# Optimization experiments

Hardware: AMD Instinct MI355X
Metric: run time of the kernel (lower is better)

Reference implementation:

```python
import jax, jax.numpy as jnp
import numpy as np

B, T, C = 2, 2048, 1024
NUM_HEADS = 16
HEAD_DIM = C // NUM_HEADS
TEMP = 1.0
LN_EPS = 1e-6


def setup_inputs() -> dict:
    key = jax.random.key(0)
    kx, kqw, kpw = jax.random.split(key, 3)
    x = jax.random.normal(kx, (B, T, C), dtype=jnp.float32)
    # causal mask, broadcastable to [B, H, T, T]
    mask = jnp.tril(jnp.ones((T, T), dtype=bool))[None, None, :, :]
    # LayerNorm params (flax defaults: scale=1, bias=0)
    ln_scale = jnp.ones((C,), dtype=jnp.float32)
    ln_bias = jnp.zeros((C,), dtype=jnp.float32)
    # xavier_uniform init for dense kernels, zero bias (torch_linear)
    lim_qkv = float(np.sqrt(6.0 / (C + 3 * C)))
    qkv_w = jax.random.uniform(kqw, (C, 3 * C), jnp.float32, -lim_qkv, lim_qkv)
    qkv_b = jnp.zeros((3 * C,), dtype=jnp.float32)
    lim_p = float(np.sqrt(6.0 / (C + C)))
    proj_w = jax.random.uniform(kpw, (C, C), jnp.float32, -lim_p, lim_p)
    proj_b = jnp.zeros((C,), dtype=jnp.float32)
    return {"x": x, "mask": mask, "ln_scale": ln_scale, "ln_bias": ln_bias,
            "qkv_w": qkv_w, "qkv_b": qkv_b, "proj_w": proj_w, "proj_b": proj_b}


def reference(x, mask, ln_scale, ln_bias, qkv_w, qkv_b, proj_w, proj_b):
    b, t, c = x.shape
    # LayerNorm (eps=1e-6, flax default)
    mu = jnp.mean(x, axis=-1, keepdims=True)
    var = jnp.mean(jnp.square(x - mu), axis=-1, keepdims=True)
    xn = (x - mu) * jax.lax.rsqrt(var + LN_EPS) * ln_scale + ln_bias
    # fused QKV projection
    qkv = xn @ qkv_w + qkv_b
    q, k, v = jnp.split(qkv, 3, axis=-1)
    q = q.reshape(b, t, NUM_HEADS, HEAD_DIM) / TEMP
    k = k.reshape(b, t, NUM_HEADS, HEAD_DIM)
    v = v.reshape(b, t, NUM_HEADS, HEAD_DIM)
    # scaled dot-product attention with mask (eval path: no dropout)
    q = q / jnp.sqrt(jnp.float32(HEAD_DIM)).astype(x.dtype)
    scores = jnp.einsum('bqhd,bkhd->bhqk', q, k)  # [B,H,T,T]
    big_neg = jnp.finfo(x.dtype).min
    scores = jnp.where(mask, scores, big_neg)
    attn_weights = jax.nn.softmax(scores, axis=-1).astype(x.dtype)
    out = jnp.einsum('bhqk,bkhd->bqhd', attn_weights, v).reshape(b, t, c)
    return out @ proj_w + proj_b
```

## Files before the change

### kernel.cpp

```cpp
#include <hip/hip_runtime.h>
#include <cstdint>
#include <math.h>

#define DEV __device__ __forceinline__

typedef unsigned int u32;
typedef unsigned short u16;
typedef __attribute__((ext_vector_type(4))) float f32x4;
typedef __attribute__((ext_vector_type(4))) u32 u32x4;
typedef __attribute__((ext_vector_type(2))) u32 u32x2;
typedef __attribute__((ext_vector_type(8))) __bf16 bf16x8;

static_assert(sizeof(bf16x8) == 16, "bf16x8 must be 16B");

static constexpr int Tn = 2048, Cn = 1024;
static constexpr float QSCALE2 = 0.125f * 1.44269504088896f;

DEV u16 f2bf_rne(float f) {
  u32 u = __builtin_bit_cast(u32, f);
  u32 r = u + 0x7fffu + ((u >> 16) & 1u);
  return (u16)(r >> 16);
}
DEV float bf2f(u16 h) {
  u32 u = ((u32)h) << 16;
  return __builtin_bit_cast(float, u);
}
DEV u32 pack2bf(float a, float b) {
  return (u32)f2bf_rne(a) | ((u32)f2bf_rne(b) << 16);
}
DEV float fexp2(float x) {
#if __has_builtin(__builtin_amdgcn_exp2f)
  return __builtin_amdgcn_exp2f(x);
#else
  return exp2f(x);
#endif
}

DEV void stage16(const void* g, void* l) {
#if __has_builtin(__builtin_amdgcn_global_load_lds)
  __builtin_amdgcn_global_load_lds(
      (__attribute__((address_space(1))) u32*)(uintptr_t)g,
      (__attribute__((address_space(3))) u32*)l, 16, 0, 0);
#else
  *(u32x4*)l = *(const u32x4*)g;
#endif
}

__global__ __launch_bounds__(256) void pre_kernel(const float* __restrict__ x,
                                                  const float* __restrict__ sc,
                                                  const float* __restrict__ bi,
                                                  u16* __restrict__ xn,
                                                  const float* __restrict__ qkv_w,
                                                  u16* __restrict__ wqkv,
                                                  const float* __restrict__ proj_w,
                                                  u16* __restrict__ wproj) {
  __shared__ float shm[32 * 33];
  int t = threadIdx.x;
  if (blockIdx.x < 4096) {
    int row = blockIdx.x;
    const float* xr = x + (size_t)row * Cn;
    f32x4 v = *(const f32x4*)(xr + t * 4);
    float s = v.x + v.y + v.z + v.w;
    float s2 = v.x * v.x + v.y * v.y + v.z * v.z + v.w * v.w;
#pragma unroll
    for (int off = 1; off < 64; off <<= 1) {
      s += __shfl_xor(s, off);
      s2 += __shfl_xor(s2, off);
    }
    if ((t & 63) == 0) {
      shm[(t >> 6) * 2] = s;
      shm[(t >> 6) * 2 + 1] = s2;
    }
    __syncthreads();
    s = shm[0] + shm[2] + shm[4] + shm[6];
    s2 = shm[1] + shm[3] + shm[5] + shm[7];
    float mean = s * (1.0f / Cn);
    float var = s2 * (1.0f / Cn) - mean * mean;
    float rstd = rsqrtf(var + 1e-6f);
    f32x4 g = *(const f32x4*)(sc + t * 4);
    f32x4 b = *(const f32x4*)(bi + t * 4);
    u32 lo = pack2bf((v.x - mean) * rstd * g.x + b.x, (v.y - mean) * rstd * g.y + b.y);
    u32 hi = pack2bf((v.z - mean) * rstd * g.z + b.z, (v.w - mean) * rstd * g.w + b.w);
    u32x2 pack = {lo, hi};
    *(u32x2*)(xn + (size_t)row * Cn + t * 4) = pack;
  } else {
    int idx = blockIdx.x - 4096;
    int bx = idx & 127, by = idx >> 7;
    const float* src;
    u16* dst;
    int Cc;
    if (bx < 96) {
      src = qkv_w; dst = wqkv; Cc = 3072;
    } else {
      src = proj_w; dst = wproj; Cc = 1024; bx -= 96;
    }
    int tx = t & 31, ty = t >> 5;
    int c0 = bx * 32, r0 = by * 32;
#pragma unroll
    for (int k = 0; k < 4; ++k)
      shm[(ty + 8 * k) * 33 + tx] = src[(size_t)(r0 + ty + 8 * k) * Cc + c0 + tx];
    __syncthreads();
#pragma unroll
    for (int k = 0; k < 4; ++k)
      dst[(size_t)(c0 + ty + 8 * k) * 1024 + r0 + tx] =
          f2bf_rne(shm[tx * 33 + ty + 8 * k]);
  }
}

template <bool OUT_F32, bool QKV>
__global__ __launch_bounds__(256, 3) void gemm_kernel(const u16* __restrict__ A,
                                                      const u16* __restrict__ Bt,
                                                      const float* __restrict__ bias,
                                                      void* __restrict__ Cout,
                                                      u16* __restrict__ vtp,
                                                      int Nsz, int Ksz) {
  __shared__ u16 As[128 * 32];
  __shared__ u16 Bs[128 * 32];
  int t = threadIdx.x;
  int l = t & 63, w = t >> 6;
  int quad = l >> 4, c16 = l & 15;
  int wm = w & 1, wn = w >> 1;
  int m0 = blockIdx.y * 128, n0 = blockIdx.x * 128;

  f32x4 acc[4][4];
#pragma unroll
  for (int mt = 0; mt < 4; ++mt)
#pragma unroll
    for (int nt = 0; nt < 4; ++nt) acc[mt][nt] = (f32x4){0.f, 0.f, 0.f, 0.f};

  for (int kk = 0; kk < Ksz; kk += 32) {
#pragma unroll
    for (int i = 0; i < 2; ++i) {
      int c = t + i * 256;
      int m = c >> 2, k8 = (c & 3) ^ ((m >> 1) & 3);
      stage16(A + (size_t)(m0 + m) * Ksz + kk + k8 * 8, (char*)As + c * 16);
    }
#pragma unroll
    for (int i = 0; i < 2; ++i) {
      int c = t + i * 256;
      int n = c >> 2, k8 = (c & 3) ^ ((n >> 1) & 3);
      stage16(Bt + (size_t)(n0 + n) * Ksz + kk + k8 * 8, (char*)Bs + c * 16);
    }
    __syncthreads();
    bf16x8 af[4], bf[4];
#pragma unroll
    for (int mt = 0; mt < 4; ++mt) {
      int m = wm * 64 + mt * 16 + c16;
      int LC = m * 4 + (quad ^ ((m >> 1) & 3));
      af[mt] = *(const bf16x8*)((const char*)As + LC * 16);
    }
#pragma unroll
    for (int nt = 0; nt < 4; ++nt) {
      int n = wn * 64 + nt * 16 + c16;
      int LC = n * 4 + (quad ^ ((n >> 1) & 3));
      bf[nt] = *(const bf16x8*)((const char*)Bs + LC * 16);
    }
#pragma unroll
    for (int mt = 0; mt < 4; ++mt)
#pragma unroll
      for (int nt = 0; nt < 4; ++nt)
        acc[mt][nt] = __builtin_amdgcn_mfma_f32_16x16x32_bf16(af[mt], bf[nt],
                                                              acc[mt][nt], 0, 0, 0);
    __syncthreads();
  }
#pragma unroll
  for (int mt = 0; mt < 4; ++mt) {
    int row = m0 + wm * 64 + mt * 16 + quad * 4;
#pragma unroll
    for (int nt = 0; nt < 4; ++nt) {
      int col = n0 + wn * 64 + nt * 16 + c16;
      float bv = bias[col];
      if (QKV && col >= 2048) {
        int hd = col - 2048;
        int bb = row >> 11, tt = row & 2047;
        u32x2 pk = {pack2bf(acc[mt][nt][0] + bv, acc[mt][nt][1] + bv),
                    pack2bf(acc[mt][nt][2] + bv, acc[mt][nt][3] + bv)};
        *(u32x2*)(vtp + ((size_t)bb * 1024 + hd) * 2048 + tt) = pk;
      } else {
        float scale = (QKV && col < 1024) ? QSCALE2 : 1.0f;
#pragma unroll
        for (int r = 0; r < 4; ++r) {
          float v = (acc[mt][nt][r] + bv) * scale;
          if (OUT_F32)
            ((float*)Cout)[(size_t)(row + r) * Nsz + col] = v;
          else
            ((u16*)Cout)[(size_t)(row + r) * Nsz + col] = f2bf_rne(v);
        }
      }
    }
  }
}

__constant__ int4 chunk_tab[24] = {
    {15, 0, 8, 0}, {15, 8, 8, 1}, {14, 0, 8, 0}, {7, 0, 8, -1},
    {14, 8, 7, 1}, {13, 0, 7, 0}, {13, 7, 7, 1}, {12, 0, 7, 0}, {6, 0, 7, -1},
    {12, 7, 6, 1}, {11, 0, 6, 0}, {11, 6, 6, 1}, {10, 0, 6, 0}, {5, 0, 6, -1},
    {10, 6, 5, 1}, {9, 0, 5, 0}, {9, 5, 5, 1}, {8, 0, 5, 0}, {4, 0, 5, -1},
    {8, 5, 4, 1}, {3, 0, 4, -1},
    {2, 0, 3, -1},
    {1, 0, 2, -1},
    {0, 0, 1, -1}};

__global__ __launch_bounds__(256, 2) void flash_kernel(const u16* __restrict__ qkv,
                                                       const u16* __restrict__ vt,
                                                       u16* __restrict__ aout,
                                                       u16* __restrict__ Op,
                                                       float* __restrict__ ml) {
  int4 ck = chunk_tab[blockIdx.x >> 5];
  int bh = blockIdx.x & 31;
  int qt = ck.x, k0 = ck.y, kend = ck.y + ck.z, half = ck.w;
  int b = bh >> 4, h = bh & 15;
  int t = threadIdx.x, l = t & 63, w = t >> 6;
  int quad = l >> 4, c16 = l & 15;
  int q0 = qt * 128;
  const u16* __restrict__ vtb = vt + (size_t)bh * 64 * 2048;
  const u16* __restrict__ kb =
      qkv + ((size_t)(b * Tn) + c16) * 3072 + Cn + h * 64 + quad * 8;

  __shared__ u16 Ps[128 * 128];

  bf16x8 qf[2][2];
#pragma unroll
  for (int nt = 0; nt < 2; ++nt)
#pragma unroll
    for (int ks = 0; ks < 2; ++ks)
      qf[nt][ks] = *(const bf16x8*)(qkv +
          (size_t)(b * Tn + q0 + w * 32 + nt * 16 + c16) * 3072 +
          h * 64 + ks * 32 + quad * 8);

  float mrow[2] = {-1e30f, -1e30f};
  float lrow[2] = {0.f, 0.f};
  f32x4 o[2][4];
#pragma unroll
  for (int mq = 0; mq < 2; ++mq)
#pragma unroll
    for (int dt = 0; dt < 4; ++dt) o[mq][dt] = (f32x4){0.f, 0.f, 0.f, 0.f};

  for (int kt = k0; kt < kend; ++kt) {
    bf16x8 vfc[4];
#pragma unroll
    for (int dt = 0; dt < 4; ++dt)
      vfc[dt] = *(const bf16x8*)(vtb + (size_t)(dt * 16 + c16) * 2048 + kt * 128 +
                                 quad * 8);
    const u16* kr = kb + (size_t)kt * 128 * 3072;
    bf16x8 ka[2][2];
#pragma unroll
    for (int p = 0; p < 2; ++p)
#pragma unroll
      for (int ks = 0; ks < 2; ++ks)
        ka[p][ks] = *(const bf16x8*)(kr + (size_t)p * 16 * 3072 + ks * 32);

    f32x4 s[8][2];
#pragma unroll
    for (int mt = 0; mt < 8; ++mt)
#pragma unroll
      for (int nt = 0; nt < 2; ++nt) s[mt][nt] = (f32x4){0.f, 0.f, 0.f, 0.f};
#pragma unroll
    for (int mt = 0; mt < 8; ++mt) {
#pragma unroll
      for (int ks = 0; ks < 2; ++ks)
#pragma unroll
        for (int nt = 0; nt < 2; ++nt)
          s[mt][nt] = __builtin_amdgcn_mfma_f32_16x16x32_bf16(
              ka[mt & 1][ks], qf[nt][ks], s[mt][nt], 0, 0, 0);
      if (mt < 6) {
#pragma unroll
        for (int ks = 0; ks < 2; ++ks)
          ka[mt & 1][ks] =
              *(const bf16x8*)(kr + (size_t)(mt + 2) * 16 * 3072 + ks * 32);
      }
    }
    if (kt == qt) {
#pragma unroll
      for (int mt = 0; mt < 8; ++mt)
#pragma unroll
        for (int nt = 0; nt < 2; ++nt)
#pragma unroll
          for (int r = 0; r < 4; ++r) {
            int key = kt * 128 + mt * 16 + quad * 4 + r;
            int q = q0 + w * 32 + nt * 16 + c16;
            if (key > q) s[mt][nt][r] = -1e30f;
          }
    }
    float alph[2];
#pragma unroll
    for (int nt = 0; nt < 2; ++nt) {
      float rm = -1e30f;
#pragma unroll
      for (int mt = 0; mt < 8; ++mt)
#pragma unroll
        for (int r = 0; r < 4; ++r) rm = fmaxf(rm, s[mt][nt][r]);
      rm = fmaxf(rm, __shfl_xor(rm, 16));
      rm = fmaxf(rm, __shfl_xor(rm, 32));
      float mnew = fmaxf(mrow[nt], rm);
      alph[nt] = fexp2(mrow[nt] - mnew);
      mrow[nt] = mnew;
      float rs = 0.f;
#pragma unroll
      for (int mt = 0; mt < 8; ++mt)
#pragma unroll
        for (int r = 0; r < 4; ++r) {
          float e = fexp2(s[mt][nt][r] - mnew);
          s[mt][nt][r] = e;
          rs += e;
        }
      rs += __shfl_xor(rs, 16);
      rs += __shfl_xor(rs, 32);
      lrow[nt] = lrow[nt] * alph[nt] + rs;
    }
#pragma unroll
    for (int mq = 0; mq < 2; ++mq)
#pragma unroll
      for (int r = 0; r < 4; ++r) {
        float a = __shfl(alph[mq], quad * 4 + r);
#pragma unroll
        for (int dt = 0; dt < 4; ++dt) o[mq][dt][r] *= a;
      }
#pragma unroll
    for (int mt = 0; mt < 8; ++mt)
#pragma unroll
      for (int nt = 0; nt < 2; ++nt) {
        int q = w * 32 + nt * 16 + c16;
        int kc = mt * 4 + quad;
        int LC = q * 32 + (kc ^ ((q & 15) << 1));
        u32x2 pk = {pack2bf(s[mt][nt][0], s[mt][nt][1]),
                    pack2bf(s[mt][nt][2], s[mt][nt][3])};
        *(u32x2*)((char*)Ps + LC * 8) = pk;
      }
#pragma unroll
    for (int ks = 0; ks < 4; ++ks) {
      bf16x8 vfn[4];
      if (ks < 3) {
#pragma unroll
        for (int dt = 0; dt < 4; ++dt)
          vfn[dt] = *(const bf16x8*)(vtb + (size_t)(dt * 16 + c16) * 2048 +
                                     kt * 128 + (ks + 1) * 32 + quad * 8);
      }
      bf16x8 pa[2];
#pragma unroll
      for (int mq = 0; mq < 2; ++mq) {
        int q = w * 32 + mq * 16 + c16;
        int kc = ks * 8 + quad * 2;
        int LC = q * 32 + (kc ^ ((q & 15) << 1));
        pa[mq] = *(const bf16x8*)((const char*)Ps + LC * 8);
      }
#pragma unroll
      for (int dt = 0; dt < 4; ++dt)
#pragma unroll
        for (int mq = 0; mq < 2; ++mq)
          o[mq][dt] = __builtin_amdgcn_mfma_f32_16x16x32_bf16(pa[mq], vfc[dt],
                                                              o[mq][dt], 0, 0, 0);
      if (ks < 3) {
#pragma unroll
        for (int dt = 0; dt < 4; ++dt) vfc[dt] = vfn[dt];
      }
    }
  }

  float linv[2] = {1.0f / lrow[0], 1.0f / lrow[1]};
  if (half < 0) {
#pragma unroll
    for (int mq = 0; mq < 2; ++mq)
#pragma unroll
      for (int r = 0; r < 4; ++r) {
        float li = __shfl(linv[mq], quad * 4 + r);
        int q = q0 + w * 32 + mq * 16 + quad * 4 + r;
#pragma unroll
        for (int dt = 0; dt < 4; ++dt)
          aout[(size_t)(b * Tn + q) * 1024 + h * 64 + dt * 16 + c16] =
              f2bf_rne(o[mq][dt][r] * li);
      }
  } else {
    int ps = ((qt - 8) * 32 + bh) * 2 + half;
#pragma unroll
    for (int mq = 0; mq < 2; ++mq)
#pragma unroll
      for (int r = 0; r < 4; ++r) {
        float li = __shfl(linv[mq], quad * 4 + r);
        int qr = w * 32 + mq * 16 + quad * 4 + r;
#pragma unroll
        for (int dt = 0; dt < 4; ++dt)
          Op[((size_t)ps * 128 + qr) * 64 + dt * 16 + c16] =
              f2bf_rne(o[mq][dt][r] * li);
      }
    if (quad == 0) {
#pragma unroll
      for (int nt = 0; nt < 2; ++nt) {
        int qr = w * 32 + nt * 16 + c16;
        ml[((size_t)ps * 128 + qr) * 2] = mrow[nt];
        ml[((size_t)ps * 128 + qr) * 2 + 1] = lrow[nt];
      }
    }
  }
}

__global__ __launch_bounds__(256) void combine_kernel(const u16* __restrict__ Op,
                                                      const float* __restrict__ ml,
                                                      u16* __restrict__ aout) {
  int qt = 8 + (blockIdx.x >> 5);
  int bh = blockIdx.x & 31;
  int b = bh >> 4, h = bh & 15;
  int ps0 = ((qt - 8) * 32 + bh) * 2;
  int d = threadIdx.x & 63, rq = threadIdx.x >> 6;
  for (int r = 0; r < 32; ++r) {
    int row = rq * 32 + r;
    float m0 = ml[((size_t)ps0 * 128 + row) * 2];
    float l0 = ml[((size_t)ps0 * 128 + row) * 2 + 1];
    float m1 = ml[((size_t)(ps0 + 1) * 128 + row) * 2];
    float l1 = ml[((size_t)(ps0 + 1) * 128 + row) * 2 + 1];
    float M = fmaxf(m0, m1);
    float w0 = fexp2(m0 - M) * l0, w1 = fexp2(m1 - M) * l1;
    float inv = 1.0f / (w0 + w1);
    float o0 = bf2f(Op[((size_t)ps0 * 128 + row) * 64 + d]);
    float o1 = bf2f(Op[((size_t)(ps0 + 1) * 128 + row) * 64 + d]);
    aout[(size_t)(b * Tn + qt * 128 + row) * 1024 + h * 64 + d] =
        f2bf_rne((w0 * o0 + w1 * o1) * inv);
  }
}

extern "C" void kernel_launch(void* const* d_in, const int* in_sizes, int n_in,
                              void* d_out, int out_size, void* d_ws, size_t ws_size,
                              hipStream_t stream) {
  const float* x = (const float*)d_in[0];
  const float* ln_s = (const float*)d_in[2];
  const float* ln_b = (const float*)d_in[3];
  const float* qkv_w = (const float*)d_in[4];
  const float* qkv_b = (const float*)d_in[5];
  const float* proj_w = (const float*)d_in[6];
  const float* proj_b = (const float*)d_in[7];
  float* out = (float*)d_out;
  char* ws = (char*)d_ws;

  u16* xn = (u16*)ws;
  u16* wqkv = (u16*)(ws + (8ull << 20));
  u16* wproj = (u16*)(ws + (14ull << 20));
  u16* qkvm = (u16*)(ws + (16ull << 20));
  u16* attn = (u16*)(ws + (40ull << 20));
  u16* vt = (u16*)(ws + (48ull << 20));
  u16* Op = (u16*)ws;
  float* ml = (float*)(ws + (8ull << 20));

  pre_kernel<<<8192, 256, 0, stream>>>(x, ln_s, ln_b, xn, qkv_w, wqkv, proj_w,
                                       wproj);
  gemm_kernel<false, true><<<dim3(24, 32), 256, 0, stream>>>(xn, wqkv, qkv_b, qkvm,
                                                             vt, 3072, 1024);
  flash_kernel<<<768, 256, 0, stream>>>(qkvm, vt, attn, Op, ml);
  combine_kernel<<<256, 256, 0, stream>>>(Op, ml, attn);
  gemm_kernel<true, false><<<dim3(8, 32), 256, 0, stream>>>(attn, wproj, proj_b, out,
                                                            nullptr, 1024, 1024);
}
```

Measured before the change: 244.4 us.

## Stage K/V tiles in shared memory for flash attention and double GEMM k-step

The flash attention kernel now copies each 128-key K tile and the matching V^T tile into swizzled LDS once per block, with the next tile's copy issued after the score MFMAs. All four waves then read fragments from LDS instead of each loading K and V directly from global memory. The GEMM kernel's k-step grows from 32 to 64, with an 8-way XOR swizzle and two MFMA sub-steps per barrier pair. This aims to cut redundant global traffic and halve GEMM barrier count, at the cost of more LDS per block (possibly lower occupancy), extra syncthreads in the attention loop, and 16 V fragments held in registers.

```diff
diff --git a/kernel.cpp b/kernel.cpp
--- a/kernel.cpp
+++ b/kernel.cpp
@@ -114,8 +114,8 @@
                                                       void* __restrict__ Cout,
                                                       u16* __restrict__ vtp,
                                                       int Nsz, int Ksz) {
-  __shared__ u16 As[128 * 32];
-  __shared__ u16 Bs[128 * 32];
+  __shared__ u16 As[128 * 64];
+  __shared__ u16 Bs[128 * 64];
   int t = threadIdx.x;
   int l = t & 63, w = t >> 6;
   int quad = l >> 4, c16 = l & 15;
@@ -128,39 +128,42 @@
 #pragma unroll
     for (int nt = 0; nt < 4; ++nt) acc[mt][nt] = (f32x4){0.f, 0.f, 0.f, 0.f};
 
-  for (int kk = 0; kk < Ksz; kk += 32) {
-#pragma unroll
-    for (int i = 0; i < 2; ++i) {
+  for (int kk = 0; kk < Ksz; kk += 64) {
+#pragma unroll
+    for (int i = 0; i < 4; ++i) {
       int c = t + i * 256;
-      int m = c >> 2, k8 = (c & 3) ^ ((m >> 1) & 3);
+      int m = c >> 3, k8 = (c & 7) ^ (m & 7);
       stage16(A + (size_t)(m0 + m) * Ksz + kk + k8 * 8, (char*)As + c * 16);
     }
 #pragma unroll
-    for (int i = 0; i < 2; ++i) {
+    for (int i = 0; i < 4; ++i) {
       int c = t + i * 256;
-      int n = c >> 2, k8 = (c & 3) ^ ((n >> 1) & 3);
+      int n = c >> 3, k8 = (c & 7) ^ (n & 7);
       stage16(Bt + (size_t)(n0 + n) * Ksz + kk + k8 * 8, (char*)Bs + c * 16);
     }
     __syncthreads();
-    bf16x8 af[4], bf[4];
-#pragma unroll
-    for (int mt = 0; mt < 4; ++mt) {
-      int m = wm * 64 + mt * 16 + c16;
-      int LC = m * 4 + (quad ^ ((m >> 1) & 3));
-      af[mt] = *(const bf16x8*)((const char*)As + LC * 16);
-    }
-#pragma unroll
-    for (int nt = 0; nt < 4; ++nt) {
-      int n = wn * 64 + nt * 16 + c16;
-      int LC = n * 4 + (quad ^ ((n >> 1) & 3));
-      bf[nt] = *(const bf16x8*)((const char*)Bs + LC * 16);
-    }
-#pragma unroll
-    for (int mt = 0; mt < 4; ++mt)
-#pragma unroll
-      for (int nt = 0; nt < 4; ++nt)
-        acc[mt][nt] = __builtin_amdgcn_mfma_f32_16x16x32_bf16(af[mt], bf[nt],
-                                                              acc[mt][nt], 0, 0, 0);
+#pragma unroll
+    for (int h = 0; h < 2; ++h) {
+      bf16x8 af[4], bf[4];
+#pragma unroll
+      for (int mt = 0; mt < 4; ++mt) {
+        int m = wm * 64 + mt * 16 + c16;
+        int LC = m * 8 + ((h * 4 + quad) ^ (m & 7));
+        af[mt] = *(const bf16x8*)((const char*)As + LC * 16);
+      }
+#pragma unroll
+      for (int nt = 0; nt < 4; ++nt) {
+        int n = wn * 64 + nt * 16 + c16;
+        int LC = n * 8 + ((h * 4 + quad) ^ (n & 7));
+        bf[nt] = *(const bf16x8*)((const char*)Bs + LC * 16);
+      }
+#pragma unroll
+      for (int mt = 0; mt < 4; ++mt)
+#pragma unroll
+        for (int nt = 0; nt < 4; ++nt)
+          acc[mt][nt] = __builtin_amdgcn_mfma_f32_16x16x32_bf16(af[mt], bf[nt],
+                                                                acc[mt][nt], 0, 0, 0);
+    }
     __syncthreads();
   }
 #pragma unroll
@@ -214,9 +217,9 @@
   int quad = l >> 4, c16 = l & 15;
   int q0 = qt * 128;
   const u16* __restrict__ vtb = vt + (size_t)bh * 64 * 2048;
-  const u16* __restrict__ kb =
-      qkv + ((size_t)(b * Tn) + c16) * 3072 + Cn + h * 64 + quad * 8;
-
+
+  __shared__ u16 Ks[128 * 64];
+  __shared__ u16 Vs[64 * 128];
   __shared__ u16 Ps[128 * 128];
 
   bf16x8 qf[2][2];
@@ -236,19 +239,32 @@
 #pragma unroll
     for (int dt = 0; dt < 4; ++dt) o[mq][dt] = (f32x4){0.f, 0.f, 0.f, 0.f};
 
+#pragma unroll
+  for (int i = 0; i < 4; ++i) {
+    int c = t + i * 256;
+    int key = c >> 3, d8 = (c & 7) ^ (key & 7);
+    stage16(qkv + (size_t)(b * Tn + k0 * 128 + key) * 3072 + Cn + h * 64 + d8 * 8,
+            (char*)Ks + c * 16);
+  }
+#pragma unroll
+  for (int i = 0; i < 4; ++i) {
+    int c = t + i * 256;
+    int d = c >> 4, k8 = (c & 15) ^ (d & 15);
+    stage16(vtb + (size_t)d * 2048 + k0 * 128 + k8 * 8, (char*)Vs + c * 16);
+  }
+
   for (int kt = k0; kt < kend; ++kt) {
-    bf16x8 vfc[4];
-#pragma unroll
-    for (int dt = 0; dt < 4; ++dt)
-      vfc[dt] = *(const bf16x8*)(vtb + (size_t)(dt * 16 + c16) * 2048 + kt * 128 +
-                                 quad * 8);
-    const u16* kr = kb + (size_t)kt * 128 * 3072;
-    bf16x8 ka[2][2];
-#pragma unroll
-    for (int p = 0; p < 2; ++p)
-#pragma unroll
-      for (int ks = 0; ks < 2; ++ks)
-        ka[p][ks] = *(const bf16x8*)(kr + (size_t)p * 16 * 3072 + ks * 32);
+    __syncthreads();
+
+    bf16x8 vf[4][4];
+#pragma unroll
+    for (int ks = 0; ks < 4; ++ks)
+#pragma unroll
+      for (int dt = 0; dt < 4; ++dt) {
+        int d = dt * 16 + c16;
+        int vc = d * 16 + ((ks * 4 + quad) ^ (d & 15));
+        vf[ks][dt] = *(const bf16x8*)((const char*)Vs + vc * 16);
+      }
 
     f32x4 s[8][2];
 #pragma unroll
@@ -258,18 +274,38 @@
 #pragma unroll
     for (int mt = 0; mt < 8; ++mt) {
 #pragma unroll
-      for (int ks = 0; ks < 2; ++ks)
+      for (int ks = 0; ks < 2; ++ks) {
+        int key = mt * 16 + c16;
+        int d8 = ks * 4 + quad;
+        int LC = key * 8 + (d8 ^ (key & 7));
+        bf16x8 kf = *(const bf16x8*)((const char*)Ks + LC * 16);
 #pragma unroll
         for (int nt = 0; nt < 2; ++nt)
-          s[mt][nt] = __builtin_amdgcn_mfma_f32_16x16x32_bf16(
-              ka[mt & 1][ks], qf[nt][ks], s[mt][nt], 0, 0, 0);
-      if (mt < 6) {
-#pragma unroll
-        for (int ks = 0; ks < 2; ++ks)
-          ka[mt & 1][ks] =
-              *(const bf16x8*)(kr + (size_t)(mt + 2) * 16 * 3072 + ks * 32);
-      }
-    }
+          s[mt][nt] = __builtin_amdgcn_mfma_f32_16x16x32_bf16(kf, qf[nt][ks],
+                                                              s[mt][nt], 0, 0, 0);
+      }
+    }
+
+    __syncthreads();
+
+    if (kt + 1 < kend) {
+#pragma unroll
+      for (int i = 0; i < 4; ++i) {
+        int c = t + i * 256;
+        int key = c >> 3, d8 = (c & 7) ^ (key & 7);
+        stage16(qkv + (size_t)(b * Tn + (kt + 1) * 128 + key) * 3072 + Cn +
+                    h * 64 + d8 * 8,
+                (char*)Ks + c * 16);
+      }
+#pragma unroll
+      for (int i = 0; i < 4; ++i) {
+        int c = t + i * 256;
+        int d = c >> 4, k8 = (c & 15) ^ (d & 15);
+        stage16(vtb + (size_t)d * 2048 + (kt + 1) * 128 + k8 * 8,
+                (char*)Vs + c * 16);
+      }
+    }
+
     if (kt == qt) {
 #pragma unroll
       for (int mt = 0; mt < 8; ++mt)
@@ -329,13 +365,6 @@
       }
 #pragma unroll
     for (int ks = 0; ks < 4; ++ks) {
-      bf16x8 vfn[4];
-      if (ks < 3) {
-#pragma unroll
-        for (int dt = 0; dt < 4; ++dt)
-          vfn[dt] = *(const bf16x8*)(vtb + (size_t)(dt * 16 + c16) * 2048 +
-                                     kt * 128 + (ks + 1) * 32 + quad * 8);
-      }
       bf16x8 pa[2];
 #pragma unroll
       for (int mq = 0; mq < 2; ++mq) {
@@ -348,12 +377,8 @@
       for (int dt = 0; dt < 4; ++dt)
 #pragma unroll
         for (int mq = 0; mq < 2; ++mq)
-          o[mq][dt] = __builtin_amdgcn_mfma_f32_16x16x32_bf16(pa[mq], vfc[dt],
+          o[mq][dt] = __builtin_amdgcn_mfma_f32_16x16x32_bf16(pa[mq], vf[ks][dt],
                                                               o[mq][dt], 0, 0, 0);
-      if (ks < 3) {
-#pragma unroll
-        for (int dt = 0; dt < 4; ++dt) vfc[dt] = vfn[dt];
-      }
     }
   }
 
```

New measurement: 223.2 us. 8.7% less time.
